# Performance work log

Hardware: AMD Instinct MI355X
Metric: run time of the kernel (lower is better)

The kernel has to match this reference:

```python
import jax, jax.numpy as jnp
import numpy as np

B, T, D, E = 4096, 64, 256, 4
H = D * E  # hidden width per token position


def setup_inputs() -> dict:
    key = jax.random.key(0)
    kx, k1, kb1, k2, kb2 = jax.random.split(key, 5)
    # torch.nn.Linear default init ~ U(-1/sqrt(fan_in), 1/sqrt(fan_in)); scaled normals are fine for a numeric reference
    x = jax.random.normal(kx, (B, T, D), dtype=jnp.float32)
    W1 = jax.random.normal(k1, (T, D, H), dtype=jnp.float32) / np.sqrt(D)
    b1 = jax.random.normal(kb1, (T, H), dtype=jnp.float32) / np.sqrt(D)
    W2 = jax.random.normal(k2, (T, H, D), dtype=jnp.float32) / np.sqrt(H)
    b2 = jax.random.normal(kb2, (T, D), dtype=jnp.float32) / np.sqrt(H)
    return {"x": x, "W1": W1, "b1": b1, "W2": W2, "b2": b2}


def reference(x, W1, b1, W2, b2):
    # Per-position MLP with distinct weights: grouped GEMM over the T axis.
    h = jnp.einsum('btd,tdh->bth', x, W1) + b1          # [B, T, H]
    h = jax.nn.gelu(h, approximate=False)                # torch GELU default = exact erf form
    out = jnp.einsum('bth,thd->btd', h, W2) + b2         # [B, T, D]
    return out
```

## Files before the change

kernel.cpp:

```cpp
#include <hip/hip_runtime.h>


typedef __bf16 bf16x8 __attribute__((ext_vector_type(8)));
typedef float  floatx4 __attribute__((ext_vector_type(4)));

__device__ __forceinline__ unsigned short f2bf(float f) {
  unsigned u = __builtin_bit_cast(unsigned, f);
  u += 0x7fffu + ((u >> 16) & 1u);
  return (unsigned short)(u >> 16);
}

__device__ __forceinline__ float gelu_exact(float v) {
  return 0.5f * v * (1.0f + erff(v * 0.70710678118654752f));
}


__global__ __launch_bounds__(256) void prep_w1(const float* __restrict__ w1,
                                               unsigned short* __restrict__ img) {
  __shared__ unsigned short simg[4096];
  const int u = threadIdx.x, bid = blockIdx.x;
  const int t = bid >> 3, kk = bid & 7;
  const float* base = w1 + (size_t)t * 262144 + (size_t)(kk * 32) * 1024;
  unsigned short* obase = img + (size_t)t * 262144 + kk * 4096;

  for (int c = 0; c < 8; ++c) {
#pragma unroll
    for (int s = 0; s < 4; ++s) {
      const int i = (s * 256 + u) * 4;
      const int dl = i >> 7, col = i & 127;
      floatx4 f = *(const floatx4*)(base + (size_t)dl * 1024 + c * 128 + col);
      const int q = dl >> 3, i8 = dl & 7;
#pragma unroll
      for (int e = 0; e < 4; ++e) {
        const int jl = col + e;
        simg[jl * 32 + ((q ^ ((jl >> 1) & 3)) << 3) + i8] = f2bf(f[e]);
      }
    }
    __syncthreads();
    *(uint4*)(obase + (size_t)c * 32768 + u * 8) = *(const uint4*)(simg + u * 8);
    *(uint4*)(obase + (size_t)c * 32768 + 2048 + u * 8) =
        *(const uint4*)(simg + 2048 + u * 8);
    __syncthreads();
  }
}

__global__ __launch_bounds__(256) void prep_w2(const float* __restrict__ w2,
                                               unsigned short* __restrict__ img) {
  __shared__ unsigned short simg[8192];
  const int u = threadIdx.x, bid = blockIdx.x;
  const int t = bid >> 3, c = bid & 7;
  const float* base = w2 + (size_t)t * 262144 + (size_t)(c * 128) * 256;
  unsigned short* obase = img + (size_t)t * 262144 + c * 32768;

  for (int kk2 = 0; kk2 < 4; ++kk2) {
#pragma unroll
    for (int s = 0; s < 8; ++s) {
      const int i = (s * 256 + u) * 4;
      const int jr = i >> 8, d = i & 255;
      floatx4 f = *(const floatx4*)(base + (size_t)(kk2 * 32 + jr) * 256 + d);
      const int q = jr >> 3, i8 = jr & 7;
#pragma unroll
      for (int e = 0; e < 4; ++e) {
        const int dd = d + e;
        simg[dd * 32 + ((q ^ ((dd >> 1) & 3)) << 3) + i8] = f2bf(f[e]);
      }
    }
    __syncthreads();
#pragma unroll
    for (int r = 0; r < 4; ++r)
      *(uint4*)(obase + (size_t)kk2 * 8192 + (r * 256 + u) * 8) =
          *(const uint4*)(simg + (r * 256 + u) * 8);
    __syncthreads();
  }
}

__global__ __launch_bounds__(256, 3) void mlp_fast2(
    const float* __restrict__ x, const unsigned short* __restrict__ w1i,
    const float* __restrict__ b1, const unsigned short* __restrict__ w2i,
    const float* __restrict__ b2, float* __restrict__ out) {

  __shared__ __attribute__((aligned(16))) unsigned char lds[53248];
  unsigned char* const xlds = lds;
  unsigned char* const hlds = lds + 32768;
  float* const b1lds = (float*)(lds + 49152);

  const int tid  = threadIdx.x;
  const int lane = tid & 63;
  const int w    = tid >> 6, wm = w >> 1, wn = w & 1;
  const int l15  = lane & 15, l4 = lane >> 4;

  const int bid = blockIdx.x;
  const int t   = (bid & 7) + 8 * (bid >> 9);
  const int b0  = ((bid >> 3) & 63) << 6;

  const unsigned char* w1t = (const unsigned char*)(w1i + (size_t)t * 262144);
  const unsigned char* w2t = (const unsigned char*)(w2i + (size_t)t * 262144);

#pragma unroll
  for (int i = 0; i < 4; ++i)
    b1lds[tid + 256 * i] = b1[t * 1024 + tid + 256 * i];

  {
    const int bl = tid >> 2, seg = tid & 3;
    const float* xr = x + ((size_t)(b0 + bl) * 64 + t) * 256 + seg * 64;
#pragma unroll
    for (int g = 0; g < 8; ++g) {
      const int d = seg * 64 + g * 8;
      floatx4 lo = *(const floatx4*)(xr + g * 8);
      floatx4 hi = *(const floatx4*)(xr + g * 8 + 4);
      union { uint4 v; unsigned short s[8]; } px;
      px.s[0] = f2bf(lo[0]); px.s[1] = f2bf(lo[1]);
      px.s[2] = f2bf(lo[2]); px.s[3] = f2bf(lo[3]);
      px.s[4] = f2bf(hi[0]); px.s[5] = f2bf(hi[1]);
      px.s[6] = f2bf(hi[2]); px.s[7] = f2bf(hi[3]);
      const int k = d >> 5, slot = (d >> 3) & 3;
      *(uint4*)(xlds + k * 4096 + bl * 64 + ((slot ^ (bl & 3)) << 4)) = px.v;
    }
  }

  floatx4 oacc[4][4];
#pragma unroll
  for (int mt = 0; mt < 4; ++mt) {
    const floatx4 bv = *(const floatx4*)(b2 + t * 256 + w * 64 + mt * 16 + l4 * 4);
#pragma unroll
    for (int nt = 0; nt < 4; ++nt) oacc[mt][nt] = bv;
  }

  __syncthreads();

  const int swf    = (l4 ^ ((lane >> 1) & 3)) << 4;
  const int w1base = ((wn * 64 + l15) << 6) + swf;
  const int w2base = ((w * 64 + l15) << 6) + swf;
  const int xbase  = (wm * 32 + l15) * 64 + ((l4 ^ (l15 & 3)) << 4);

  bf16x8 bcur[4];
#pragma unroll
  for (int nt = 0; nt < 4; ++nt)
    bcur[nt] = *(const bf16x8*)(w1t + w1base + nt * 1024);

#pragma unroll 1
  for (int c = 0; c < 8; ++c) {
    floatx4 hacc[2][4];
#pragma unroll
    for (int nt = 0; nt < 4; ++nt) {
      const float bv = b1lds[c * 128 + wn * 64 + nt * 16 + l15];
      const floatx4 bb = {bv, bv, bv, bv};
      hacc[0][nt] = bb; hacc[1][nt] = bb;
    }

#pragma unroll
    for (int k = 0; k < 8; ++k) {
      const int s = c * 8 + k;
      const unsigned char* nsrc =
          w1t + (size_t)((s < 63 ? s + 1 : 63) * 8192);
      bf16x8 bnxt[4];
#pragma unroll
      for (int nt = 0; nt < 4; ++nt)
        bnxt[nt] = *(const bf16x8*)(nsrc + w1base + nt * 1024);
      const bf16x8 xf0 = *(const bf16x8*)(xlds + k * 4096 + xbase);
      const bf16x8 xf1 = *(const bf16x8*)(xlds + k * 4096 + xbase + 1024);
      __builtin_amdgcn_s_setprio(1);
#pragma unroll
      for (int nt = 0; nt < 4; ++nt) {
        hacc[0][nt] = __builtin_amdgcn_mfma_f32_16x16x32_bf16(
            xf0, bcur[nt], hacc[0][nt], 0, 0, 0);
        hacc[1][nt] = __builtin_amdgcn_mfma_f32_16x16x32_bf16(
            xf1, bcur[nt], hacc[1][nt], 0, 0, 0);
      }
      __builtin_amdgcn_s_setprio(0);
#pragma unroll
      for (int nt = 0; nt < 4; ++nt) bcur[nt] = bnxt[nt];
    }

#pragma unroll
    for (int mt = 0; mt < 2; ++mt)
#pragma unroll
      for (int nt = 0; nt < 4; ++nt) {
        const int jl = wn * 64 + nt * 16 + l15;
        const int q  = jl >> 3;
        const int jo = (jl & 7) * 2;
#pragma unroll
        for (int r = 0; r < 4; ++r) {
          const float g = gelu_exact(hacc[mt][nt][r]);
          const int b = wm * 32 + mt * 16 + l4 * 4 + r;
          *(unsigned short*)(hlds + b * 256 + ((q ^ (b & 7)) * 16) + jo) = f2bf(g);
        }
      }

    bf16x8 acur[4];
    {
      const unsigned char* asrc = w2t + (size_t)(c * 4) * 16384;
#pragma unroll
      for (int mt = 0; mt < 4; ++mt)
        acur[mt] = *(const bf16x8*)(asrc + w2base + mt * 1024);
    }

    asm volatile("s_waitcnt lgkmcnt(0)" ::: "memory");
    __builtin_amdgcn_s_barrier();
    asm volatile("" ::: "memory");

#pragma unroll
    for (int k2 = 0; k2 < 4; ++k2) {
      bf16x8 anxt[4];
      if (k2 < 3) {
        const unsigned char* nsrc2 = w2t + (size_t)(c * 4 + k2 + 1) * 16384;
#pragma unroll
        for (int mt = 0; mt < 4; ++mt)
          anxt[mt] = *(const bf16x8*)(nsrc2 + w2base + mt * 1024);
      }
      bf16x8 hfr[4];
#pragma unroll
      for (int nt = 0; nt < 4; ++nt)
        hfr[nt] = *(const bf16x8*)(hlds + (nt * 16 + l15) * 256 +
                                   (((k2 * 4 + l4) ^ (lane & 7)) * 16));
      __builtin_amdgcn_s_setprio(1);
#pragma unroll
      for (int mt = 0; mt < 4; ++mt)
#pragma unroll
        for (int nt = 0; nt < 4; ++nt)
          oacc[mt][nt] = __builtin_amdgcn_mfma_f32_16x16x32_bf16(
              acur[mt], hfr[nt], oacc[mt][nt], 0, 0, 0);
      __builtin_amdgcn_s_setprio(0);
      if (k2 < 3) {
#pragma unroll
        for (int mt = 0; mt < 4; ++mt) acur[mt] = anxt[mt];
      }
    }

    asm volatile("s_waitcnt lgkmcnt(0)" ::: "memory");
    __builtin_amdgcn_s_barrier();
    asm volatile("" ::: "memory");
  }

#pragma unroll
  for (int mt = 0; mt < 4; ++mt) {
    const int d = w * 64 + mt * 16 + l4 * 4;
#pragma unroll
    for (int nt = 0; nt < 4; ++nt) {
      const int b = b0 + nt * 16 + l15;
      *(floatx4*)(out + ((size_t)b * 64 + t) * 256 + d) = oacc[mt][nt];
    }
  }
}

__global__ __launch_bounds__(256, 2) void mlp_kernel(
    const float* __restrict__ x, const float* __restrict__ w1,
    const float* __restrict__ b1, const float* __restrict__ w2,
    const float* __restrict__ b2, float* __restrict__ out) {

  __shared__ __attribute__((aligned(16))) unsigned char lds[40960];
  unsigned char* const w1img = lds;
  unsigned char* const w2img = lds + 8192;
  unsigned char* const hlds  = lds + 24576;

  const int tid  = threadIdx.x;
  const int lane = tid & 63;
  const int w    = tid >> 6;
  const int wm   = w >> 1;
  const int wn   = w & 1;
  const int l15  = lane & 15;
  const int l4   = lane >> 4;

  const int bid  = blockIdx.x;
  const int t    = (bid & 7) + 8 * (bid >> 9);
  const int b0   = ((bid >> 3) & 63) << 6;

  const float* w1t = w1 + (size_t)t * 262144;
  const float* w2t = w2 + (size_t)t * 262144;

  const int jl_s   = tid & 127;
  const int half_s = tid >> 7;
  const int P_s    = half_s ^ ((jl_s >> 2) & 1);
  const int sw2s   = (tid >> 1) & 3;

  bf16x8 xfrag[2][8];
#pragma unroll
  for (int mt = 0; mt < 2; ++mt) {
    const int b = b0 + wm * 32 + mt * 16 + l15;
    const float* xb = x + ((size_t)b * 64 + t) * 256 + l4 * 8;
#pragma unroll
    for (int kk = 0; kk < 8; ++kk) {
      floatx4 lo = *(const floatx4*)(xb + kk * 32);
      floatx4 hi = *(const floatx4*)(xb + kk * 32 + 4);
      union { bf16x8 v; unsigned short s[8]; } px;
      px.s[0] = f2bf(lo[0]); px.s[1] = f2bf(lo[1]);
      px.s[2] = f2bf(lo[2]); px.s[3] = f2bf(lo[3]);
      px.s[4] = f2bf(hi[0]); px.s[5] = f2bf(hi[1]);
      px.s[6] = f2bf(hi[2]); px.s[7] = f2bf(hi[3]);
      xfrag[mt][kk] = px.v;
    }
  }

  floatx4 oacc[4][4];
#pragma unroll
  for (int mt = 0; mt < 4; ++mt) {
    const floatx4 bv = *(const floatx4*)(b2 + t * 256 + w * 64 + mt * 16 + l4 * 4);
#pragma unroll
    for (int nt = 0; nt < 4; ++nt) oacc[mt][nt] = bv;
  }

  const int swf    = (l4 ^ ((lane >> 1) & 3)) << 4;
  const int w1base = ((wn * 64 + l15) << 6) + swf;
  const int w2base = ((w * 64 + l15) << 6) + swf;

#pragma unroll 1
  for (int c = 0; c < 8; ++c) {
    floatx4 hacc[2][4];
#pragma unroll
    for (int nt = 0; nt < 4; ++nt) {
      const float bv = b1[t * 1024 + c * 128 + wn * 64 + nt * 16 + l15];
      const floatx4 bb = {bv, bv, bv, bv};
      hacc[0][nt] = bb; hacc[1][nt] = bb;
    }

#pragma unroll
    for (int kk = 0; kk < 8; ++kk) {
      float f[16];
      const float* src = w1t + (size_t)(kk * 32 + half_s * 16) * 1024 + c * 128 + jl_s;
#pragma unroll
      for (int u = 0; u < 16; ++u) f[u] = src[(size_t)u * 1024];

      __syncthreads();
      union { uint4 v; unsigned short s[8]; } pk[2];
#pragma unroll
      for (int u = 0; u < 16; ++u) pk[u >> 3].s[u & 7] = f2bf(f[u]);
#pragma unroll
      for (int p = 0; p < 2; ++p) {
        const int m = 2 * P_s + p;
        const int s = (p ^ (jl_s >> 1)) & 1;
        *(uint4*)(w1img + jl_s * 64 + m * 16) = pk[s].v;
      }
      __syncthreads();

      bf16x8 bfrag[4];
#pragma unroll
      for (int nt = 0; nt < 4; ++nt)
        bfrag[nt] = *(const bf16x8*)(w1img + w1base + nt * 1024);
#pragma unroll
      for (int mt = 0; mt < 2; ++mt)
#pragma unroll
        for (int nt = 0; nt < 4; ++nt)
          hacc[mt][nt] = __builtin_amdgcn_mfma_f32_16x16x32_bf16(
              xfrag[mt][kk], bfrag[nt], hacc[mt][nt], 0, 0, 0);
    }

#pragma unroll
    for (int mt = 0; mt < 2; ++mt) {
#pragma unroll
      for (int nt = 0; nt < 4; ++nt) {
        const int jl = wn * 64 + nt * 16 + l15;
        const int q  = jl >> 3;
        const int jo = (jl & 7) * 2;
#pragma unroll
        for (int r = 0; r < 4; ++r) {
          const float g = gelu_exact(hacc[mt][nt][r]);
          const int b = wm * 32 + mt * 16 + l4 * 4 + r;
          *(unsigned short*)(hlds + b * 256 + ((q ^ (b & 7)) * 16) + jo) = f2bf(g);
        }
      }
    }

#pragma unroll
    for (int kk2 = 0; kk2 < 4; ++kk2) {
      float g2[32];
      const float* src2 = w2t + (size_t)(c * 128 + kk2 * 32) * 256 + tid;
#pragma unroll
      for (int v = 0; v < 32; ++v) g2[v] = src2[(size_t)v * 256];

      __syncthreads();
      union { uint4 v; unsigned short s[8]; } pk2[4];
#pragma unroll
      for (int v = 0; v < 32; ++v) pk2[v >> 3].s[v & 7] = f2bf(g2[v]);
#pragma unroll
      for (int p = 0; p < 4; ++p) {
        const int m = (p + (tid >> 1)) & 3;
        const int q = m ^ sw2s;
        *(uint4*)(w2img + tid * 64 + m * 16) = pk2[q].v;
      }
      __syncthreads();

      bf16x8 afrag[4];
#pragma unroll
      for (int mt = 0; mt < 4; ++mt)
        afrag[mt] = *(const bf16x8*)(w2img + w2base + mt * 1024);
      bf16x8 hfrag[4];
#pragma unroll
      for (int nt = 0; nt < 4; ++nt)
        hfrag[nt] = *(const bf16x8*)(hlds + (nt * 16 + l15) * 256 +
                                     (((kk2 * 4 + l4) ^ (lane & 7)) * 16));
#pragma unroll
      for (int mt = 0; mt < 4; ++mt)
#pragma unroll
        for (int nt = 0; nt < 4; ++nt)
          oacc[mt][nt] = __builtin_amdgcn_mfma_f32_16x16x32_bf16(
              afrag[mt], hfrag[nt], oacc[mt][nt], 0, 0, 0);
    }
  }

#pragma unroll
  for (int mt = 0; mt < 4; ++mt) {
    const int d = w * 64 + mt * 16 + l4 * 4;
#pragma unroll
    for (int nt = 0; nt < 4; ++nt) {
      const int b = b0 + nt * 16 + l15;
      *(floatx4*)(out + ((size_t)b * 64 + t) * 256 + d) = oacc[mt][nt];
    }
  }
}

extern "C" void kernel_launch(void* const* d_in, const int* in_sizes, int n_in,
                              void* d_out, int out_size, void* d_ws, size_t ws_size,
                              hipStream_t stream) {
  const float* x  = (const float*)d_in[0];
  const float* W1 = (const float*)d_in[1];
  const float* b1 = (const float*)d_in[2];
  const float* W2 = (const float*)d_in[3];
  const float* b2 = (const float*)d_in[4];
  float* out = (float*)d_out;

  const size_t need = 67108864;
  if (d_ws != nullptr && ws_size >= need) {
    unsigned short* w1img = (unsigned short*)d_ws;
    unsigned short* w2img = (unsigned short*)((char*)d_ws + 33554432);
    prep_w1<<<512, 256, 0, stream>>>(W1, w1img);
    prep_w2<<<512, 256, 0, stream>>>(W2, w2img);
    mlp_fast2<<<4096, 256, 0, stream>>>(x, w1img, b1, w2img, b2, out);
  } else {
    mlp_kernel<<<4096, 256, 0, stream>>>(x, W1, b1, W2, b2, out);
  }
}
```

Before: 1.029 ms.

## Deepen weight prefetch pipeline across GEMM phases and use fast GELU approximation

Reworks the register-level prefetch of weight fragments. W1 fragments are now loaded two steps ahead, and W2 fragments for the second GEMM are issued during the tail of the first GEMM. The next chunk's W1 fragments are issued during the second GEMM, and the end-of-chunk barrier is moved before the h store. Exact erf GELU is also replaced with an Abramowitz-Stegun polynomial using hardware rcp/exp. The aim is to hide global load latency and cut transcendental cost, at the price of more live registers (risking occupancy at 3 waves/SIMD) and a small accuracy loss in GELU.

Measured after the change: 1.242 ms. 1.21x slower.

```diff
diff --git a/kernel.cpp b/kernel.cpp
--- a/kernel.cpp
+++ b/kernel.cpp
@@ -12,6 +12,28 @@
 
 __device__ __forceinline__ float gelu_exact(float v) {
   return 0.5f * v * (1.0f + erff(v * 0.70710678118654752f));
+}
+
+__device__ __forceinline__ float gelu_fast(float v) {
+  const float av = __builtin_fabsf(v);
+  const float z  = av * 0.70710678118654752f;
+  float t;
+  {
+    const float d = __builtin_fmaf(z, 0.3275911f, 1.0f);
+    asm("v_rcp_f32 %0, %1" : "=v"(t) : "v"(d));
+  }
+  float p = __builtin_fmaf(t, 1.061405429f, -1.453152027f);
+  p = __builtin_fmaf(t, p, 1.421413741f);
+  p = __builtin_fmaf(t, p, -0.284496736f);
+  p = __builtin_fmaf(t, p, 0.254829592f);
+  p = p * t;
+  float e;
+  {
+    const float m = -(z * z) * 1.4426950408889634f;
+    asm("v_exp_f32 %0, %1" : "=v"(e) : "v"(m));
+  }
+  const float relu = 0.5f * (v + av);
+  return __builtin_fmaf(-0.5f * av * p, e, relu);
 }
 
 
@@ -74,7 +96,7 @@
   }
 }
 
-__global__ __launch_bounds__(256, 3) void mlp_fast2(
+__global__ __launch_bounds__(256, 3) void mlp_fast3(
     const float* __restrict__ x, const unsigned short* __restrict__ w1i,
     const float* __restrict__ b1, const unsigned short* __restrict__ w2i,
     const float* __restrict__ b2, float* __restrict__ out) {
@@ -133,10 +155,14 @@
   const int w2base = ((w * 64 + l15) << 6) + swf;
   const int xbase  = (wm * 32 + l15) * 64 + ((l4 ^ (l15 & 3)) << 4);
 
-  bf16x8 bcur[4];
-#pragma unroll
-  for (int nt = 0; nt < 4; ++nt)
-    bcur[nt] = *(const bf16x8*)(w1t + w1base + nt * 1024);
+  bf16x8 bA[4], bB[4], bC[4];
+  bf16x8 aP[4], aQ[4];
+
+#pragma unroll
+  for (int nt = 0; nt < 4; ++nt) {
+    bA[nt] = *(const bf16x8*)(w1t + 0 * 8192 + w1base + nt * 1024);
+    bB[nt] = *(const bf16x8*)(w1t + 1 * 8192 + w1base + nt * 1024);
+  }
 
 #pragma unroll 1
   for (int c = 0; c < 8; ++c) {
@@ -150,27 +176,45 @@
 
 #pragma unroll
     for (int k = 0; k < 8; ++k) {
-      const int s = c * 8 + k;
-      const unsigned char* nsrc =
-          w1t + (size_t)((s < 63 ? s + 1 : 63) * 8192);
-      bf16x8 bnxt[4];
-#pragma unroll
-      for (int nt = 0; nt < 4; ++nt)
-        bnxt[nt] = *(const bf16x8*)(nsrc + w1base + nt * 1024);
+      if (k < 6) {
+        const unsigned char* nsrc = w1t + (size_t)(c * 8 + k + 2) * 8192;
+#pragma unroll
+        for (int nt = 0; nt < 4; ++nt)
+          bC[nt] = *(const bf16x8*)(nsrc + w1base + nt * 1024);
+      } else if (k == 6) {
+        const unsigned char* asrc = w2t + (size_t)(c * 4 + 0) * 16384;
+#pragma unroll
+        for (int mt = 0; mt < 4; ++mt)
+          aP[mt] = *(const bf16x8*)(asrc + w2base + mt * 1024);
+      } else {
+        const unsigned char* asrc = w2t + (size_t)(c * 4 + 1) * 16384;
+#pragma unroll
+        for (int mt = 0; mt < 4; ++mt)
+          aQ[mt] = *(const bf16x8*)(asrc + w2base + mt * 1024);
+      }
       const bf16x8 xf0 = *(const bf16x8*)(xlds + k * 4096 + xbase);
       const bf16x8 xf1 = *(const bf16x8*)(xlds + k * 4096 + xbase + 1024);
       __builtin_amdgcn_s_setprio(1);
 #pragma unroll
       for (int nt = 0; nt < 4; ++nt) {
         hacc[0][nt] = __builtin_amdgcn_mfma_f32_16x16x32_bf16(
-            xf0, bcur[nt], hacc[0][nt], 0, 0, 0);
+            xf0, bA[nt], hacc[0][nt], 0, 0, 0);
         hacc[1][nt] = __builtin_amdgcn_mfma_f32_16x16x32_bf16(
-            xf1, bcur[nt], hacc[1][nt], 0, 0, 0);
+            xf1, bA[nt], hacc[1][nt], 0, 0, 0);
       }
       __builtin_amdgcn_s_setprio(0);
-#pragma unroll
-      for (int nt = 0; nt < 4; ++nt) bcur[nt] = bnxt[nt];
-    }
+      if (k < 6) {
+#pragma unroll
+        for (int nt = 0; nt < 4; ++nt) { bA[nt] = bB[nt]; bB[nt] = bC[nt]; }
+      } else if (k == 6) {
+#pragma unroll
+        for (int nt = 0; nt < 4; ++nt) bA[nt] = bB[nt];
+      }
+    }
+
+    asm volatile("" ::: "memory");
+    __builtin_amdgcn_s_barrier();
+    asm volatile("" ::: "memory");
 
 #pragma unroll
     for (int mt = 0; mt < 2; ++mt)
@@ -181,55 +225,64 @@
         const int jo = (jl & 7) * 2;
 #pragma unroll
         for (int r = 0; r < 4; ++r) {
-          const float g = gelu_exact(hacc[mt][nt][r]);
+          const float g = gelu_fast(hacc[mt][nt][r]);
           const int b = wm * 32 + mt * 16 + l4 * 4 + r;
           *(unsigned short*)(hlds + b * 256 + ((q ^ (b & 7)) * 16) + jo) = f2bf(g);
         }
       }
 
-    bf16x8 acur[4];
-    {
-      const unsigned char* asrc = w2t + (size_t)(c * 4) * 16384;
-#pragma unroll
-      for (int mt = 0; mt < 4; ++mt)
-        acur[mt] = *(const bf16x8*)(asrc + w2base + mt * 1024);
-    }
-
     asm volatile("s_waitcnt lgkmcnt(0)" ::: "memory");
     __builtin_amdgcn_s_barrier();
     asm volatile("" ::: "memory");
 
 #pragma unroll
     for (int k2 = 0; k2 < 4; ++k2) {
-      bf16x8 anxt[4];
-      if (k2 < 3) {
-        const unsigned char* nsrc2 = w2t + (size_t)(c * 4 + k2 + 1) * 16384;
-#pragma unroll
-        for (int mt = 0; mt < 4; ++mt)
-          anxt[mt] = *(const bf16x8*)(nsrc2 + w2base + mt * 1024);
-      }
       bf16x8 hfr[4];
 #pragma unroll
       for (int nt = 0; nt < 4; ++nt)
         hfr[nt] = *(const bf16x8*)(hlds + (nt * 16 + l15) * 256 +
                                    (((k2 * 4 + l4) ^ (lane & 7)) * 16));
       __builtin_amdgcn_s_setprio(1);
-#pragma unroll
-      for (int mt = 0; mt < 4; ++mt)
-#pragma unroll
-        for (int nt = 0; nt < 4; ++nt)
-          oacc[mt][nt] = __builtin_amdgcn_mfma_f32_16x16x32_bf16(
-              acur[mt], hfr[nt], oacc[mt][nt], 0, 0, 0);
+      if ((k2 & 1) == 0) {
+#pragma unroll
+        for (int mt = 0; mt < 4; ++mt)
+#pragma unroll
+          for (int nt = 0; nt < 4; ++nt)
+            oacc[mt][nt] = __builtin_amdgcn_mfma_f32_16x16x32_bf16(
+                aP[mt], hfr[nt], oacc[mt][nt], 0, 0, 0);
+      } else {
+#pragma unroll
+        for (int mt = 0; mt < 4; ++mt)
+#pragma unroll
+          for (int nt = 0; nt < 4; ++nt)
+            oacc[mt][nt] = __builtin_amdgcn_mfma_f32_16x16x32_bf16(
+                aQ[mt], hfr[nt], oacc[mt][nt], 0, 0, 0);
+      }
       __builtin_amdgcn_s_setprio(0);
-      if (k2 < 3) {
-#pragma unroll
-        for (int mt = 0; mt < 4; ++mt) acur[mt] = anxt[mt];
-      }
-    }
-
-    asm volatile("s_waitcnt lgkmcnt(0)" ::: "memory");
-    __builtin_amdgcn_s_barrier();
-    asm volatile("" ::: "memory");
+      if (k2 == 0) {
+        const unsigned char* asrc = w2t + (size_t)(c * 4 + 2) * 16384;
+#pragma unroll
+        for (int mt = 0; mt < 4; ++mt)
+          aP[mt] = *(const bf16x8*)(asrc + w2base + mt * 1024);
+        if (c < 7) {
+          const unsigned char* nsrc = w1t + (size_t)((c + 1) * 8) * 8192;
+#pragma unroll
+          for (int nt = 0; nt < 4; ++nt)
+            bA[nt] = *(const bf16x8*)(nsrc + w1base + nt * 1024);
+        }
+      } else if (k2 == 1) {
+        const unsigned char* asrc = w2t + (size_t)(c * 4 + 3) * 16384;
+#pragma unroll
+        for (int mt = 0; mt < 4; ++mt)
+          aQ[mt] = *(const bf16x8*)(asrc + w2base + mt * 1024);
+        if (c < 7) {
+          const unsigned char* nsrc = w1t + (size_t)((c + 1) * 8 + 1) * 8192;
+#pragma unroll
+          for (int nt = 0; nt < 4; ++nt)
+            bB[nt] = *(const bf16x8*)(nsrc + w1base + nt * 1024);
+        }
+      }
+    }
   }
 
 #pragma unroll
@@ -424,7 +477,7 @@
     unsigned short* w2img = (unsigned short*)((char*)d_ws + 33554432);
     prep_w1<<<512, 256, 0, stream>>>(W1, w1img);
     prep_w2<<<512, 256, 0, stream>>>(W2, w2img);
-    mlp_fast2<<<4096, 256, 0, stream>>>(x, w1img, b1, w2img, b2, out);
+    mlp_fast3<<<4096, 256, 0, stream>>>(x, w1img, b1, w2img, b2, out);
   } else {
     mlp_kernel<<<4096, 256, 0, stream>>>(x, W1, b1, W2, b2, out);
   }
```
